# Kernel tuning notes

Measured on AMD Instinct MI355X. Metric: run time of the kernel, lower is better.

## Reference

```python
import jax, jax.numpy as jnp
import numpy as np

B, S, D, E, H, TOPK = 4, 1024, 512, 8, 1536, 2
NORM_EPS = 1e-5

def _ln(x, w, b, eps=1e-5):
    m = jnp.mean(x, -1, keepdims=True)
    v = jnp.var(x, -1, keepdims=True)  # biased var, as torch LayerNorm
    return (x - m) * jax.lax.rsqrt(v + eps) * w + b

def _modulate(x, shift, scale):
    return x * (1 + scale[:, None, :]) + shift[:, None, :]

def setup_inputs() -> dict:
    key = jax.random.key(0)
    ks = jax.random.split(key, 14)
    s = 0.02
    return dict(
        x=jax.random.normal(ks[0], (B, S, D), jnp.float32),
        c=jax.random.normal(ks[1], (B, D), jnp.float32),
        W_ada=jax.random.normal(ks[2], (D, 6 * D), jnp.float32) * s,
        b_ada=jax.random.normal(ks[3], (6 * D,), jnp.float32) * 0.1,
        Wq=jax.random.normal(ks[4], (D, D), jnp.float32) * s,
        Wk=jax.random.normal(ks[5], (D, D), jnp.float32) * s,
        Wv=jax.random.normal(ks[6], (D, D), jnp.float32) * s,
        Wo=jax.random.normal(ks[7], (D, D), jnp.float32) * s,
        qn_w=jnp.ones((D,), jnp.float32), qn_b=jnp.zeros((D,), jnp.float32),
        kn_w=jnp.ones((D,), jnp.float32), kn_b=jnp.zeros((D,), jnp.float32),
        an_w=jnp.ones((D,), jnp.float32), an_b=jnp.zeros((D,), jnp.float32),
        fn_w=jnp.ones((D,), jnp.float32), fn_b=jnp.zeros((D,), jnp.float32),
        Wr=jax.random.normal(ks[8], (D, E), jnp.float32) * s,
        br=jnp.zeros((E,), jnp.float32),
        W1=jax.random.normal(ks[9], (E, D, H), jnp.float32) * s,
        W2=jax.random.normal(ks[10], (E, H, D), jnp.float32) * s,
        W3=jax.random.normal(ks[11], (E, D, H), jnp.float32) * s,
    )

def reference(x, c, W_ada, b_ada, Wq, Wk, Wv, Wo, qn_w, qn_b, kn_w, kn_b,
              an_w, an_b, fn_w, fn_b, Wr, br, W1, W2, W3):
    # adaLN conditioning: SiLU -> Linear -> 6 chunks
    mods = jax.nn.silu(c) @ W_ada + b_ada          # (B, 6D)
    sh_msa, sc_msa, g_msa, sh_mlp, sc_mlp, g_mlp = jnp.split(mods, 6, axis=1)

    # Attention (source attends over the FEATURE dim: scores are (B, D, D))
    h = _modulate(_ln(x, an_w, an_b, NORM_EPS), sh_msa, sc_msa)
    q = _ln(h @ Wq, qn_w, qn_b)
    k = _ln(h @ Wk, kn_w, kn_b)
    v = h @ Wv
    scores = jnp.einsum('bsd,bse->bde', q, k)      # (B, D, D), no 1/sqrt scale (as source)
    A = jax.nn.softmax(scores, axis=-1)
    attn = jnp.einsum('bde,bse->bsd', A, v) @ Wo   # (B, S, D)
    x = x + g_msa[:, None, :] * attn

    # MoE feed-forward (top-2 routing; output REPLACES x, no residual/gate per source)
    xm = _modulate(_ln(x, fn_w, fn_b, NORM_EPS), sh_mlp, sc_mlp)
    logits = xm @ Wr + br                          # (B, S, E)
    # F.normalize default dim=1 -> L2 normalize over the SEQUENCE axis (faithful)
    nrm = jnp.sqrt(jnp.sum(logits * logits, axis=1, keepdims=True))
    logits = logits / jnp.maximum(nrm, 1e-12)
    probs = jax.nn.softmax(logits, axis=-1)        # (B, S, E)
    vals, idx = jax.lax.top_k(probs, TOPK)

    T = B * S
    xf = xm.reshape(T, D)
    # dense combine weights: zero for unselected experts (same math as gather/scatter-add)
    wden = jnp.zeros((T, E), xf.dtype).at[jnp.arange(T)[:, None], idx.reshape(T, TOPK)].set(vals.reshape(T, TOPK))
    h1 = jnp.einsum('td,edh->teh', xf, W1)
    h3 = jnp.einsum('td,edh->teh', xf, W3)
    y = jnp.einsum('teh,ehd->ted', jnp.sin(h1) * h3, W2)  # sin-gated FFN per expert
    moe = jnp.einsum('ted,te->td', y, wden).reshape(B, S, D)

    avg = probs.mean(axis=0)                       # mean over batch dim only (faithful): (S, E)
    aux = jnp.sum((1.0 / E - avg) ** 2)
    return moe, aux
```

## Files before the change

kernel.cpp:

```cpp
#include <hip/hip_runtime.h>
#include <math.h>

#define NB 4
#define NS 1024
#define ND 512
#define NE 8
#define NH 1536
#define NT 4096
#define D6 3072

typedef _Float16 half_t;
typedef _Float16 f16x8 __attribute__((ext_vector_type(8)));
typedef _Float16 f16x4 __attribute__((ext_vector_type(4)));
typedef float    f32x4 __attribute__((ext_vector_type(4)));

#define LDC 136
#define TM_MAX 71

__device__ __forceinline__ void gld16(const void* g, void* l) {
  __builtin_amdgcn_global_load_lds((const __attribute__((address_space(1))) char*)g,
                                   (__attribute__((address_space(3))) char*)l, 16, 0, 0);
}

__device__ __forceinline__ int xcd_chunk(int bid, int nwg) {
  int xcd = bid & 7, ixc = bid >> 3;
  int q = nwg >> 3, r = nwg & 7;
  return (xcd < r ? xcd * (q + 1) : r * (q + 1) + (xcd - r) * q) + ixc;
}

__device__ __forceinline__ int resolve_tile(const int* __restrict__ offs, int t,
                                            int& e_out, int& m0_out) {
  int acc = 0, found = 0, ee = 0, mm = 0;
  #pragma unroll
  for (int q = 0; q < NE; ++q) {
    int ne_q = offs[q + 1] - offs[q];
    int te = (ne_q + 127) >> 7;
    if (!found && t < acc + te) { ee = q; mm = (t - acc) << 7; found = 1; }
    acc += te;
  }
  e_out = ee; m0_out = mm;
  return found;
}

__global__ __launch_bounds__(256) void k_ada(const float* __restrict__ c,
    const float* __restrict__ Wada, const float* __restrict__ bada,
    float* __restrict__ mods)
{
  __shared__ float sc[ND];
  __shared__ float part[256];
  int tid = threadIdx.x;
  int blk = blockIdx.x;
  int o0 = blk * 32;
  int b = o0 / D6;
  int j0 = o0 - b * D6;
  for (int d = tid; d < ND; d += 256) {
    float v = c[b * ND + d];
    sc[d] = v / (1.f + expf(-v));
  }
  __syncthreads();
  int j = j0 + (tid & 31);
  int kc = tid >> 5;
  float acc = 0.f;
  #pragma unroll 8
  for (int d = kc * 64; d < kc * 64 + 64; ++d)
    acc += sc[d] * Wada[(size_t)d * D6 + j];
  part[tid] = acc;
  __syncthreads();
  if (tid < 32) {
    float r = bada[j0 + tid];
    #pragma unroll
    for (int k = 0; k < 8; ++k) r += part[tid + 32 * k];
    mods[b * D6 + j0 + tid] = r;
  }
}

__global__ __launch_bounds__(256) void k_lnmod(const float* X, int xstride,
    float* Yf, half_t* Yh, half_t* Yl, int ystride,
    const float* __restrict__ w, const float* __restrict__ b,
    const float* __restrict__ mods, int sh_off, int sc_off,
    const float* __restrict__ Wr, const float* __restrict__ br,
    float* __restrict__ logits)
{
  __shared__ float red[16];
  __shared__ float red2[32];
  int tid = threadIdx.x;
  int row = blockIdx.x;
  int batch = row >> 10;
  const float* xr = X + (size_t)row * xstride;
  float x0 = xr[tid], x1 = xr[tid + 256];
  float s = x0 + x1, q = x0 * x0 + x1 * x1;
  #pragma unroll
  for (int off = 32; off > 0; off >>= 1) { s += __shfl_down(s, off, 64); q += __shfl_down(q, off, 64); }
  if ((tid & 63) == 0) { red[tid >> 6] = s; red[8 + (tid >> 6)] = q; }
  __syncthreads();
  if (tid == 0) {
    float S = red[0] + red[1] + red[2] + red[3];
    float Q = red[8] + red[9] + red[10] + red[11];
    float mean = S * (1.f / (float)ND);
    float var = Q * (1.f / (float)ND) - mean * mean;
    red[0] = mean; red[1] = rsqrtf(var + 1e-5f);
  }
  __syncthreads();
  float mean = red[0], rstd = red[1];
  int d0 = tid, d1 = tid + 256;
  float y0 = (x0 - mean) * rstd * w[d0] + b[d0];
  float y1 = (x1 - mean) * rstd * w[d1] + b[d1];
  if (mods) {
    const float* mb = mods + batch * D6;
    y0 = y0 * (1.f + mb[sc_off + d0]) + mb[sh_off + d0];
    y1 = y1 * (1.f + mb[sc_off + d1]) + mb[sh_off + d1];
  }
  size_t o0 = (size_t)row * ystride + d0, o1 = (size_t)row * ystride + d1;
  if (Yf) { Yf[o0] = y0; Yf[o1] = y1; }
  if (Yh) {
    half_t h0 = (half_t)y0, h1 = (half_t)y1;
    Yh[o0] = h0; Yh[o1] = h1;
    if (Yl) { Yl[o0] = (half_t)(y0 - (float)h0); Yl[o1] = (half_t)(y1 - (float)h1); }
  }
  if (Wr) {
    float p[8];
    float4 wa = *(const float4*)(Wr + d0 * 8);
    float4 wb = *(const float4*)(Wr + d0 * 8 + 4);
    float4 wc = *(const float4*)(Wr + d1 * 8);
    float4 wd = *(const float4*)(Wr + d1 * 8 + 4);
    p[0] = y0 * wa.x + y1 * wc.x; p[1] = y0 * wa.y + y1 * wc.y;
    p[2] = y0 * wa.z + y1 * wc.z; p[3] = y0 * wa.w + y1 * wc.w;
    p[4] = y0 * wb.x + y1 * wd.x; p[5] = y0 * wb.y + y1 * wd.y;
    p[6] = y0 * wb.z + y1 * wd.z; p[7] = y0 * wb.w + y1 * wd.w;
    #pragma unroll
    for (int off = 32; off > 0; off >>= 1)
      #pragma unroll
      for (int e = 0; e < 8; ++e) p[e] += __shfl_down(p[e], off, 64);
    if ((tid & 63) == 0) {
      #pragma unroll
      for (int e = 0; e < 8; ++e) red2[(tid >> 6) * 8 + e] = p[e];
    }
    __syncthreads();
    if (tid < 8)
      logits[(size_t)row * 8 + tid] = red2[tid] + red2[8 + tid] + red2[16 + tid]
                                    + red2[24 + tid] + br[tid];
  }
}

__global__ __launch_bounds__(256) void k_lnt(const float* __restrict__ QKV,
    const float* __restrict__ qw, const float* __restrict__ qb,
    const float* __restrict__ kw, const float* __restrict__ kb,
    half_t* __restrict__ H0, half_t* __restrict__ L0)
{
  __shared__ float stats[32][2];
  __shared__ float tile[32][33];
  int h = blockIdx.y;
  int s0 = blockIdx.x * 32;
  const float* w = h ? kw : qw;
  const float* b = h ? kb : qb;
  half_t* outH = H0 + (size_t)h * 4194304;
  half_t* outL = L0 + (size_t)h * 4194304;
  int col0 = h * 512;
  int tid = threadIdx.x;
  {
    int r = tid >> 3, c8 = tid & 7;
    const float* xr = QKV + (size_t)(s0 + r) * 1536 + col0 + c8 * 64;
    float s = 0.f, q = 0.f;
    #pragma unroll
    for (int i = 0; i < 16; ++i) {
      float4 v = *(const float4*)(xr + i * 4);
      s += v.x + v.y + v.z + v.w;
      q += v.x * v.x + v.y * v.y + v.z * v.z + v.w * v.w;
    }
    #pragma unroll
    for (int off = 4; off > 0; off >>= 1) {
      s += __shfl_down(s, off, 8);
      q += __shfl_down(q, off, 8);
    }
    if (c8 == 0) {
      float mean = s * (1.f / 512.f);
      float var = q * (1.f / 512.f) - mean * mean;
      stats[r][0] = mean;
      stats[r][1] = rsqrtf(var + 1e-5f);
    }
  }
  __syncthreads();
  int r = tid >> 5, c = tid & 31;
  #pragma unroll 1
  for (int ct = 0; ct < 16; ++ct) {
    int cb = ct * 32;
    #pragma unroll
    for (int p = 0; p < 4; ++p) {
      int rr = r + p * 8;
      float v = QKV[(size_t)(s0 + rr) * 1536 + col0 + cb + c];
      tile[rr][c] = (v - stats[rr][0]) * stats[rr][1] * w[cb + c] + b[cb + c];
    }
    __syncthreads();
    #pragma unroll
    for (int p = 0; p < 4; ++p) {
      int rr = r + p * 8;
      float v = tile[c][rr];
      half_t hh = (half_t)v;
      size_t o = (size_t)(cb + rr) * NT + s0 + c;
      outH[o] = hh;
      outL[o] = (half_t)(v - (float)hh);
    }
    __syncthreads();
  }
}

__global__ __launch_bounds__(256) void k_wsplit4(const float* __restrict__ Wq,
    const float* __restrict__ Wk, const float* __restrict__ Wv,
    const float* __restrict__ Wo, half_t* __restrict__ outH, half_t* __restrict__ outL)
{
  __shared__ float tile[32][33];
  int z = blockIdx.z;
  const float* W = (z == 0) ? Wq : (z == 1) ? Wk : (z == 2) ? Wv : Wo;
  int rowoff = z * 512;
  int k0 = blockIdx.x * 32, n0 = blockIdx.y * 32;
  int tid = threadIdx.x;
  int r = tid >> 5, c = tid & 31;
  #pragma unroll
  for (int p = 0; p < 4; ++p)
    tile[r + p * 8][c] = W[(size_t)(k0 + r + p * 8) * ND + n0 + c];
  __syncthreads();
  #pragma unroll
  for (int p = 0; p < 4; ++p) {
    float v = tile[c][r + p * 8];
    half_t h = (half_t)v;
    size_t o = (size_t)(rowoff + n0 + r + p * 8) * ND + k0 + c;
    outH[o] = h; outL[o] = (half_t)(v - (float)h);
  }
}

template<int MODE>
__global__ __launch_bounds__(256, 2) void k_gemm_hl(
    const half_t* __restrict__ Ah, const half_t* __restrict__ Al, long long sAz,
    const half_t* __restrict__ Bh, const half_t* __restrict__ Bl, long long sBz,
    int lda, int ldb, int K,
    float* __restrict__ Cf, half_t* __restrict__ Ch, half_t* __restrict__ Cl,
    long long sCz, int ldc,
    const float* __restrict__ xres, const float* __restrict__ mods,
    half_t* __restrict__ vh, half_t* __restrict__ vl)
{
  int z = blockIdx.z;
  int m0 = blockIdx.x * 128, n0 = blockIdx.y * 128;
  __shared__ __align__(16) char smem[65536];
  half_t* Sh = (half_t*)smem;
  int tid = threadIdx.x;
  int lane = tid & 63, w = tid >> 6;
  int wm = (w >> 1) * 64, wn = (w & 1) * 64;
  int qd = lane >> 4, md = lane & 15;
  int rA0 = tid >> 2;
  int sw = (((tid & 3) ^ ((tid >> 3) & 3)) << 3);

  const half_t* pAh0 = Ah + z * sAz + (size_t)(m0 + rA0) * lda + sw;
  const half_t* pAh1 = pAh0 + (size_t)64 * lda;
  const half_t* pAl0 = Al + z * sAz + (size_t)(m0 + rA0) * lda + sw;
  const half_t* pAl1 = pAl0 + (size_t)64 * lda;
  const half_t* pBh0 = Bh + z * sBz + (size_t)(n0 + rA0) * ldb + sw;
  const half_t* pBh1 = pBh0 + (size_t)64 * ldb;
  const half_t* pBl0 = Bl + z * sBz + (size_t)(n0 + rA0) * ldb + sw;
  const half_t* pBl1 = pBl0 + (size_t)64 * ldb;

  char* dAh = smem + w * 1024;
  char* dAl = smem + 16384 + w * 1024;
  char* dBh = smem + 32768 + w * 1024;
  char* dBl = smem + 49152 + w * 1024;

  f32x4 acc[4][4];
  #pragma unroll
  for (int i = 0; i < 4; ++i)
    #pragma unroll
    for (int j = 0; j < 4; ++j)
      #pragma unroll
      for (int p = 0; p < 4; ++p) acc[i][j][p] = 0.f;

  int swq  = ((qd ^ ((md >> 1) & 3)) << 3);
  int aoff = (wm + md) * 32 + swq;
  int boff = (wn + md) * 32 + swq;

#define GEMM_STAGE(p, kk) do { int kb_ = (kk); int pb_ = (p) * 8192;         \
    gld16(pAh0 + kb_, dAh + pb_); gld16(pAh1 + kb_, dAh + pb_ + 4096);       \
    gld16(pAl0 + kb_, dAl + pb_); gld16(pAl1 + kb_, dAl + pb_ + 4096);       \
    gld16(pBh0 + kb_, dBh + pb_); gld16(pBh1 + kb_, dBh + pb_ + 4096);       \
    gld16(pBl0 + kb_, dBl + pb_); gld16(pBl1 + kb_, dBl + pb_ + 4096); } while (0)

  int iters = K >> 5;
  GEMM_STAGE(0, 0);
  int cur = 0;
  #pragma unroll 1
  for (int it = 0; it < iters; ++it) {
    if (it + 1 < iters) {
      GEMM_STAGE(cur ^ 1, (it + 1) * 32);
      asm volatile("s_waitcnt vmcnt(8)\ns_barrier" ::: "memory");
    } else {
      asm volatile("s_waitcnt vmcnt(0)\ns_barrier" ::: "memory");
    }
    const half_t* Ash = Sh + cur * 4096;
    const half_t* Asl = Sh + 8192  + cur * 4096;
    const half_t* Bsh = Sh + 16384 + cur * 4096;
    const half_t* Bsl = Sh + 24576 + cur * 4096;
    f16x8 ah[4], al[4], bh[4], bl[4];
    #pragma unroll
    for (int i = 0; i < 4; ++i) {
      ah[i] = *(const f16x8*)(Ash + aoff + i * 512);
      al[i] = *(const f16x8*)(Asl + aoff + i * 512);
    }
    #pragma unroll
    for (int j = 0; j < 4; ++j) {
      bh[j] = *(const f16x8*)(Bsh + boff + j * 512);
      bl[j] = *(const f16x8*)(Bsl + boff + j * 512);
    }
    __builtin_amdgcn_s_setprio(1);
    #pragma unroll
    for (int i = 0; i < 4; ++i)
      #pragma unroll
      for (int j = 0; j < 4; ++j) {
        acc[i][j] = __builtin_amdgcn_mfma_f32_16x16x32_f16(ah[i], bh[j], acc[i][j], 0, 0, 0);
        acc[i][j] = __builtin_amdgcn_mfma_f32_16x16x32_f16(ah[i], bl[j], acc[i][j], 0, 0, 0);
        acc[i][j] = __builtin_amdgcn_mfma_f32_16x16x32_f16(al[i], bh[j], acc[i][j], 0, 0, 0);
      }
    __builtin_amdgcn_s_setprio(0);
    asm volatile("s_barrier" ::: "memory");
    cur ^= 1;
  }
#undef GEMM_STAGE

  if (MODE == 1) {
    half_t* Cs = (half_t*)smem;
    __syncthreads();
    #pragma unroll
    for (int i = 0; i < 4; ++i)
      #pragma unroll
      for (int j = 0; j < 4; ++j)
        #pragma unroll
        for (int p = 0; p < 4; ++p)
          Cs[(wm + 16 * i + qd * 4 + p) * LDC + wn + 16 * j + md] = (half_t)acc[i][j][p];
    __syncthreads();
    #pragma unroll
    for (int it2 = 0; it2 < 8; ++it2) {
      int chunk = it2 * 256 + tid;
      int r = chunk >> 4, c8 = (chunk & 15) * 8;
      *(f16x8*)(Ch + z * sCz + (size_t)(m0 + r) * ldc + n0 + c8) = *(const f16x8*)(Cs + r * LDC + c8);
    }
    __syncthreads();
    #pragma unroll
    for (int i = 0; i < 4; ++i)
      #pragma unroll
      for (int j = 0; j < 4; ++j)
        #pragma unroll
        for (int p = 0; p < 4; ++p) {
          float v = acc[i][j][p];
          half_t h = (half_t)v;
          Cs[(wm + 16 * i + qd * 4 + p) * LDC + wn + 16 * j + md] = (half_t)(v - (float)h);
        }
    __syncthreads();
    #pragma unroll
    for (int it2 = 0; it2 < 8; ++it2) {
      int chunk = it2 * 256 + tid;
      int r = chunk >> 4, c8 = (chunk & 15) * 8;
      *(f16x8*)(Cl + z * sCz + (size_t)(m0 + r) * ldc + n0 + c8) = *(const f16x8*)(Cs + r * LDC + c8);
    }
  } else if (MODE == 3 && n0 >= 1024) {
    #pragma unroll
    for (int i = 0; i < 4; ++i)
      #pragma unroll
      for (int p = 0; p < 4; ++p) {
        int r = m0 + wm + 16 * i + qd * 4 + p;
        int vc = n0 - 1024 + wn + md;
        half_t* hp = vh + (size_t)r * ND + vc;
        half_t* lp = vl + (size_t)r * ND + vc;
        #pragma unroll
        for (int j = 0; j < 4; ++j) {
          float v = acc[i][j][p];
          half_t h = (half_t)v;
          hp[16 * j] = h;
          lp[16 * j] = (half_t)(v - (float)h);
        }
      }
  } else {
    #pragma unroll
    for (int i = 0; i < 4; ++i)
      #pragma unroll
      for (int p = 0; p < 4; ++p) {
        int r = m0 + wm + 16 * i + qd * 4 + p;
        float* cp = Cf + z * sCz + (size_t)r * ldc + n0 + wn + md;
        if (MODE == 2) {
          int batch = r >> 10;
          const float* mb = mods + batch * D6 + 2 * ND;
          const float* xp = xres + (size_t)r * ldc + n0 + wn + md;
          #pragma unroll
          for (int j = 0; j < 4; ++j) {
            int col = wn + md + 16 * j;
            cp[16 * j] = xp[16 * j] + mb[n0 + col] * acc[i][j][p];
          }
        } else {
          #pragma unroll
          for (int j = 0; j < 4; ++j) cp[16 * j] = acc[i][j][p];
        }
      }
  }
}

__global__ __launch_bounds__(256) void k_softmax512_sum4(const float* __restrict__ SC4,
    half_t* __restrict__ Ph, half_t* __restrict__ Pl)
{
  __shared__ float red[16];
  int tid = threadIdx.x;
  int row = blockIdx.x;
  int b = row >> 9, d = row & 511;
  const float* r0 = SC4 + ((size_t)(b * 4 + 0) << 18) + (size_t)d * ND;
  const float* r1 = SC4 + ((size_t)(b * 4 + 1) << 18) + (size_t)d * ND;
  const float* r2 = SC4 + ((size_t)(b * 4 + 2) << 18) + (size_t)d * ND;
  const float* r3 = SC4 + ((size_t)(b * 4 + 3) << 18) + (size_t)d * ND;
  float x0 = r0[tid] + r1[tid] + r2[tid] + r3[tid];
  float x1 = r0[tid + 256] + r1[tid + 256] + r2[tid + 256] + r3[tid + 256];
  float m = fmaxf(x0, x1);
  #pragma unroll
  for (int off = 32; off > 0; off >>= 1) m = fmaxf(m, __shfl_down(m, off, 64));
  if ((tid & 63) == 0) red[tid >> 6] = m;
  __syncthreads();
  if (tid == 0) red[0] = fmaxf(fmaxf(red[0], red[1]), fmaxf(red[2], red[3]));
  __syncthreads();
  m = red[0];
  float e0 = expf(x0 - m), e1 = expf(x1 - m);
  float s = e0 + e1;
  #pragma unroll
  for (int off = 32; off > 0; off >>= 1) s += __shfl_down(s, off, 64);
  if ((tid & 63) == 0) red[8 + (tid >> 6)] = s;
  __syncthreads();
  if (tid == 0) red[8] = red[8] + red[9] + red[10] + red[11];
  __syncthreads();
  float inv = 1.f / red[8];
  float p0 = e0 * inv, p1 = e1 * inv;
  size_t base = (size_t)row * ND;
  half_t h0 = (half_t)p0, h1 = (half_t)p1;
  Ph[base + tid] = h0;       Pl[base + tid] = (half_t)(p0 - (float)h0);
  Ph[base + tid + 256] = h1; Pl[base + tid + 256] = (half_t)(p1 - (float)h1);
}

__global__ __launch_bounds__(256) void k_colnorm(const float* __restrict__ logits,
    float* __restrict__ nrm)
{
  __shared__ float red[8];
  int tid = threadIdx.x;
  int b = blockIdx.x >> 3, e = blockIdx.x & 7;
  float acc = 0.f;
  for (int s = tid; s < NS; s += 256) {
    float l = logits[((size_t)(b << 10) + s) * NE + e];
    acc += l * l;
  }
  #pragma unroll
  for (int off = 32; off > 0; off >>= 1) acc += __shfl_down(acc, off, 64);
  if ((tid & 63) == 0) red[tid >> 6] = acc;
  __syncthreads();
  if (tid == 0) nrm[b * NE + e] = sqrtf(red[0] + red[1] + red[2] + red[3]);
}

__global__ __launch_bounds__(1024) void k_route(const float* __restrict__ logits,
    const float* __restrict__ nrm,
    float* __restrict__ wsel, int* __restrict__ offs_g,
    int* __restrict__ list, int* __restrict__ inv,
    float* __restrict__ outAux)
{
  __shared__ unsigned char sisel[8192];
  __shared__ int cw[8][16][8];
  __shared__ int soffs[9];
  __shared__ float snrm[32];
  __shared__ float auxred[16];
  int tid = threadIdx.x;
  int lane = tid & 63, wv = tid >> 6;
  if (tid < 32) snrm[tid] = fmaxf(nrm[tid], 1e-12f);
  __syncthreads();
  float asum[8];
  #pragma unroll
  for (int e = 0; e < 8; ++e) asum[e] = 0.f;
  #pragma unroll 1
  for (int c = 0; c < 4; ++c) {
    int t = c * 1024 + tid;
    int b = t >> 10;
    float p[8];
    float4 l0 = *(const float4*)(logits + (size_t)t * 8);
    float4 l1 = *(const float4*)(logits + (size_t)t * 8 + 4);
    p[0] = l0.x / snrm[b * 8 + 0]; p[1] = l0.y / snrm[b * 8 + 1];
    p[2] = l0.z / snrm[b * 8 + 2]; p[3] = l0.w / snrm[b * 8 + 3];
    p[4] = l1.x / snrm[b * 8 + 4]; p[5] = l1.y / snrm[b * 8 + 5];
    p[6] = l1.z / snrm[b * 8 + 6]; p[7] = l1.w / snrm[b * 8 + 7];
    float mx = p[0];
    #pragma unroll
    for (int e = 1; e < 8; ++e) mx = fmaxf(mx, p[e]);
    float s = 0.f;
    #pragma unroll
    for (int e = 0; e < 8; ++e) { p[e] = expf(p[e] - mx); s += p[e]; }
    float invs = 1.f / s;
    #pragma unroll
    for (int e = 0; e < 8; ++e) { p[e] *= invs; asum[e] += p[e]; }
    int i1 = 0;
    #pragma unroll
    for (int e = 1; e < 8; ++e) if (p[e] > p[i1]) i1 = e;
    int i2 = (i1 == 0) ? 1 : 0;
    #pragma unroll
    for (int e = 0; e < 8; ++e) if (e != i1 && p[e] > p[i2]) i2 = e;
    wsel[t * 2] = p[i1]; wsel[t * 2 + 1] = p[i2];
    sisel[t * 2] = (unsigned char)i1; sisel[t * 2 + 1] = (unsigned char)i2;
  }
  float aloc = 0.f;
  #pragma unroll
  for (int e = 0; e < 8; ++e) {
    float d = 0.125f - asum[e] * 0.25f;
    aloc += d * d;
  }
  #pragma unroll
  for (int off = 32; off > 0; off >>= 1) aloc += __shfl_down(aloc, off, 64);
  if (lane == 0) auxred[wv] = aloc;
  __syncthreads();
  if (tid == 0) {
    float a = 0.f;
    #pragma unroll
    for (int k = 0; k < 16; ++k) a += auxred[k];
    *outAux = a;
  }
  #pragma unroll 1
  for (int c = 0; c < 8; ++c) {
    int em = sisel[c * 1024 + tid];
    #pragma unroll
    for (int e = 0; e < 8; ++e) {
      unsigned long long mask = __ballot(em == e);
      if (lane == 0) cw[c][wv][e] = (int)__popcll(mask);
    }
  }
  __syncthreads();
  if (tid < 8) {
    int e = tid, run = 0;
    for (int c = 0; c < 8; ++c)
      for (int w2 = 0; w2 < 16; ++w2) { int v = cw[c][w2][e]; cw[c][w2][e] = run; run += v; }
    soffs[e] = run;
  }
  __syncthreads();
  if (tid == 0) {
    int a = 0;
    #pragma unroll
    for (int e = 0; e < 8; ++e) { int v = soffs[e]; soffs[e] = a; a += v; }
    soffs[8] = a;
  }
  __syncthreads();
  if (tid < 9) offs_g[tid] = soffs[tid];
  #pragma unroll 1
  for (int c = 0; c < 8; ++c) {
    int idx = c * 1024 + tid;
    int em = sisel[idx];
    int rk = 0;
    #pragma unroll
    for (int e = 0; e < 8; ++e) {
      unsigned long long mask = __ballot(em == e);
      if (em == e) rk = (int)__popcll(mask & ((1ull << lane) - 1ull));
    }
    int slot = soffs[em] + cw[c][wv][em] + rk;
    list[slot] = idx >> 1;
    inv[idx] = slot;
  }
}

__global__ __launch_bounds__(256) void k_tcast13(const float* __restrict__ W1,
    const float* __restrict__ W3, half_t* __restrict__ W1t, half_t* __restrict__ W3t)
{
  __shared__ float tile[64][68];
  int z = blockIdx.z;
  int sel = z >> 3, e = z & 7;
  const float* We = (sel ? W3 : W1) + (size_t)e * ND * NH;
  half_t* Wte = (sel ? W3t : W1t) + (size_t)e * ND * NH;
  int k0 = blockIdx.x * 64, n0 = blockIdx.y * 64;
  int tid = threadIdx.x;
  int r = tid >> 4, c4 = tid & 15;
  #pragma unroll
  for (int p = 0; p < 4; ++p) {
    int row = r + p * 16;
    float4 v = *(const float4*)(We + (size_t)(k0 + row) * NH + n0 + c4 * 4);
    tile[row][c4 * 4 + 0] = v.x; tile[row][c4 * 4 + 1] = v.y;
    tile[row][c4 * 4 + 2] = v.z; tile[row][c4 * 4 + 3] = v.w;
  }
  __syncthreads();
  #pragma unroll
  for (int p = 0; p < 4; ++p) {
    int orow = r + p * 16;
    f16x4 h;
    #pragma unroll
    for (int i = 0; i < 4; ++i) h[i] = (half_t)tile[c4 * 4 + i][orow];
    *(f16x4*)(Wte + (size_t)(n0 + orow) * ND + k0 + c4 * 4) = h;
  }
}

__global__ __launch_bounds__(256) void k_tcastW2(const float* __restrict__ W,
    half_t* __restrict__ Wt)
{
  __shared__ float tile[64][68];
  const float* We = W + (size_t)blockIdx.z * NH * ND;
  half_t* Wte = Wt + (size_t)blockIdx.z * NH * ND;
  int k0 = blockIdx.x * 64, n0 = blockIdx.y * 64;
  int tid = threadIdx.x;
  int r = tid >> 4, c4 = tid & 15;
  #pragma unroll
  for (int p = 0; p < 4; ++p) {
    int row = r + p * 16;
    float4 v = *(const float4*)(We + (size_t)(k0 + row) * ND + n0 + c4 * 4);
    tile[row][c4 * 4 + 0] = v.x; tile[row][c4 * 4 + 1] = v.y;
    tile[row][c4 * 4 + 2] = v.z; tile[row][c4 * 4 + 3] = v.w;
  }
  __syncthreads();
  #pragma unroll
  for (int p = 0; p < 4; ++p) {
    int orow = r + p * 16;
    f16x4 h;
    #pragma unroll
    for (int i = 0; i < 4; ++i) h[i] = (half_t)tile[c4 * 4 + i][orow];
    *(f16x4*)(Wte + (size_t)(n0 + orow) * NH + k0 + c4 * 4) = h;
  }
}

__global__ __launch_bounds__(256, 3) void k_ffn_fused(const half_t* __restrict__ xmh,
    const half_t* __restrict__ W1t, const half_t* __restrict__ W3t,
    const int* __restrict__ list, const int* __restrict__ offs,
    half_t* __restrict__ gate)
{
  int bx = xcd_chunk(blockIdx.x, TM_MAX * 12);
  int n0 = (bx % 12) * 128;
  int t  = bx / 12;
  int e, m0;
  if (!resolve_tile(offs, t, e, m0)) return;
  int base = offs[e], ne = offs[e + 1] - base;

  __shared__ __align__(16) char smem[49664];
  half_t* Sh = (half_t*)smem;
  int* rowt = (int*)(smem + 49152);
  int tid = threadIdx.x;
  if (tid < 128) {
    int rr = m0 + tid;
    rowt[tid] = (rr < ne) ? list[base + rr] : 0;
  }
  __syncthreads();

  int lane = tid & 63, w = tid >> 6;
  int wm = (w >> 1) * 64, wn = (w & 1) * 64;
  int qd = lane >> 4, md = lane & 15;
  int rA0 = tid >> 2;
  int sw = (((tid & 3) ^ ((tid >> 3) & 3)) << 3);
  int tok0 = rowt[rA0], tok1 = rowt[rA0 + 64];

  const half_t* gA0  = xmh + (size_t)tok0 * ND + sw;
  const half_t* gA1  = xmh + (size_t)tok1 * ND + sw;
  const half_t* gB10 = W1t + ((size_t)e * NH + n0 + rA0) * ND + sw;
  const half_t* gB11 = gB10 + (size_t)64 * ND;
  const half_t* gB30 = W3t + ((size_t)e * NH + n0 + rA0) * ND + sw;
  const half_t* gB31 = gB30 + (size_t)64 * ND;

  char* dA  = smem + w * 1024;
  char* dB1 = smem + 16384 + w * 1024;
  char* dB3 = smem + 32768 + w * 1024;

  f32x4 acc1[4][4], acc3[4][4];
  #pragma unroll
  for (int i = 0; i < 4; ++i)
    #pragma unroll
    for (int j = 0; j < 4; ++j)
      #pragma unroll
      for (int p = 0; p < 4; ++p) { acc1[i][j][p] = 0.f; acc3[i][j][p] = 0.f; }

  int swq  = ((qd ^ ((md >> 1) & 3)) << 3);
  int aoff = (wm + md) * 32 + swq;
  int boff = (wn + md) * 32 + swq;

#define FFN_STAGE(p, kk) do { int kb_ = (kk); int pb_ = (p) * 8192;          \
    gld16(gA0  + kb_, dA  + pb_); gld16(gA1  + kb_, dA  + pb_ + 4096);       \
    gld16(gB10 + kb_, dB1 + pb_); gld16(gB11 + kb_, dB1 + pb_ + 4096);       \
    gld16(gB30 + kb_, dB3 + pb_); gld16(gB31 + kb_, dB3 + pb_ + 4096); } while (0)

  FFN_STAGE(0, 0);
  int cur = 0;
  #pragma unroll 1
  for (int it = 0; it < 16; ++it) {
    if (it + 1 < 16) {
      FFN_STAGE(cur ^ 1, (it + 1) * 32);
      asm volatile("s_waitcnt vmcnt(6)\ns_barrier" ::: "memory");
    } else {
      asm volatile("s_waitcnt vmcnt(0)\ns_barrier" ::: "memory");
    }
    const half_t* As  = Sh + cur * 4096;
    const half_t* B1s = Sh + 8192  + cur * 4096;
    const half_t* B3s = Sh + 16384 + cur * 4096;
    f16x8 a[4];
    #pragma unroll
    for (int i = 0; i < 4; ++i) a[i] = *(const f16x8*)(As + aoff + i * 512);
    __builtin_amdgcn_s_setprio(1);
    #pragma unroll
    for (int j = 0; j < 4; ++j) {
      f16x8 b1 = *(const f16x8*)(B1s + boff + j * 512);
      f16x8 b3 = *(const f16x8*)(B3s + boff + j * 512);
      #pragma unroll
      for (int i = 0; i < 4; ++i) {
        acc1[i][j] = __builtin_amdgcn_mfma_f32_16x16x32_f16(a[i], b1, acc1[i][j], 0, 0, 0);
        acc3[i][j] = __builtin_amdgcn_mfma_f32_16x16x32_f16(a[i], b3, acc3[i][j], 0, 0, 0);
      }
    }
    __builtin_amdgcn_s_setprio(0);
    asm volatile("s_barrier" ::: "memory");
    cur ^= 1;
  }
#undef FFN_STAGE

  half_t* Cs = (half_t*)smem;
  #pragma unroll
  for (int i = 0; i < 4; ++i)
    #pragma unroll
    for (int j = 0; j < 4; ++j)
      #pragma unroll
      for (int p = 0; p < 4; ++p) {
        int rr = wm + 16 * i + qd * 4 + p;
        int cc = wn + 16 * j + md;
        Cs[rr * LDC + cc] = (half_t)(__sinf(acc1[i][j][p]) * acc3[i][j][p]);
      }
  __syncthreads();
  #pragma unroll
  for (int it = 0; it < 8; ++it) {
    int chunk = it * 256 + tid;
    int rr = chunk >> 4, c8 = (chunk & 15) * 8;
    if (m0 + rr < ne) {
      *(f16x8*)(gate + (size_t)(base + m0 + rr) * NH + n0 + c8) = *(const f16x8*)(Cs + rr * LDC + c8);
    }
  }
}

__global__ __launch_bounds__(256, 4) void k_moe2_mfma(const half_t* __restrict__ gate,
    const half_t* __restrict__ W2t, const int* __restrict__ offs,
    float* __restrict__ P)
{
  int bx = xcd_chunk(blockIdx.x, TM_MAX * 4);
  int n0 = (bx & 3) * 128;
  int t = bx >> 2;
  int e, m0;
  if (!resolve_tile(offs, t, e, m0)) return;
  int base = offs[e], ne = offs[e + 1] - base;

  __shared__ __align__(16) char smem[32768];
  half_t* Sh = (half_t*)smem;
  int tid = threadIdx.x;
  int lane = tid & 63, w = tid >> 6;
  int wm = (w >> 1) * 64, wn = (w & 1) * 64;
  int qd = lane >> 4, md = lane & 15;
  int rA0 = tid >> 2;
  int sw = (((tid & 3) ^ ((tid >> 3) & 3)) << 3);

  int ar0 = m0 + rA0;      if (ar0 >= ne) ar0 = ne - 1;
  int ar1 = m0 + rA0 + 64; if (ar1 >= ne) ar1 = ne - 1;
  const half_t* gA0 = gate + (size_t)(base + ar0) * NH + sw;
  const half_t* gA1 = gate + (size_t)(base + ar1) * NH + sw;
  const half_t* gB0 = W2t + ((size_t)e * ND + n0 + rA0) * NH + sw;
  const half_t* gB1 = gB0 + (size_t)64 * NH;

  char* dA = smem + w * 1024;
  char* dB = smem + 16384 + w * 1024;

  f32x4 acc[4][4];
  #pragma unroll
  for (int i = 0; i < 4; ++i)
    #pragma unroll
    for (int j = 0; j < 4; ++j)
      #pragma unroll
      for (int p = 0; p < 4; ++p) acc[i][j][p] = 0.f;

  int swq  = ((qd ^ ((md >> 1) & 3)) << 3);
  int aoff = (wm + md) * 32 + swq;
  int boff = (wn + md) * 32 + swq;

#define MOE2_STAGE(p, kk) do { int kb_ = (kk); int pb_ = (p) * 8192;         \
    gld16(gA0 + kb_, dA + pb_); gld16(gA1 + kb_, dA + pb_ + 4096);           \
    gld16(gB0 + kb_, dB + pb_); gld16(gB1 + kb_, dB + pb_ + 4096); } while (0)

  MOE2_STAGE(0, 0);
  int cur = 0;
  #pragma unroll 1
  for (int it = 0; it < 48; ++it) {
    if (it + 1 < 48) {
      MOE2_STAGE(cur ^ 1, (it + 1) * 32);
      asm volatile("s_waitcnt vmcnt(4)\ns_barrier" ::: "memory");
    } else {
      asm volatile("s_waitcnt vmcnt(0)\ns_barrier" ::: "memory");
    }
    const half_t* As = Sh + cur * 4096;
    const half_t* Bs = Sh + 8192 + cur * 4096;
    f16x8 a[4], b[4];
    #pragma unroll
    for (int i = 0; i < 4; ++i) a[i] = *(const f16x8*)(As + aoff + i * 512);
    #pragma unroll
    for (int j = 0; j < 4; ++j) b[j] = *(const f16x8*)(Bs + boff + j * 512);
    __builtin_amdgcn_s_setprio(1);
    #pragma unroll
    for (int j = 0; j < 4; ++j)
      #pragma unroll
      for (int i = 0; i < 4; ++i)
        acc[i][j] = __builtin_amdgcn_mfma_f32_16x16x32_f16(a[i], b[j], acc[i][j], 0, 0, 0);
    __builtin_amdgcn_s_setprio(0);
    asm volatile("s_barrier" ::: "memory");
    cur ^= 1;
  }
#undef MOE2_STAGE

  #pragma unroll
  for (int i = 0; i < 4; ++i)
    #pragma unroll
    for (int p = 0; p < 4; ++p) {
      int gr = m0 + wm + 16 * i + qd * 4 + p;
      if (gr < ne) {
        float* pp = P + (size_t)(base + gr) * ND + n0 + wn + md;
        #pragma unroll
        for (int j = 0; j < 4; ++j)
          pp[16 * j] = acc[i][j][p];
      }
    }
}

__global__ __launch_bounds__(256) void k_moe_reduce(const float* __restrict__ P,
    const int* __restrict__ inv, const float* __restrict__ wsel,
    float* __restrict__ out)
{
  int i = blockIdx.x * 256 + threadIdx.x;
  int t = i >> 7, d4 = i & 127;
  int s1 = inv[t * 2], s2 = inv[t * 2 + 1];
  float w1 = wsel[t * 2], w2 = wsel[t * 2 + 1];
  const float4* P4 = (const float4*)P;
  float4 a = P4[(size_t)s1 * 128 + d4];
  float4 b = P4[(size_t)s2 * 128 + d4];
  float4 o;
  o.x = w1 * a.x + w2 * b.x;
  o.y = w1 * a.y + w2 * b.y;
  o.z = w1 * a.z + w2 * b.z;
  o.w = w1 * a.w + w2 * b.w;
  ((float4*)out)[i] = o;
}

static const size_t BO_MODS  = 0;
static const size_t BO_HH    = 65536;
static const size_t BO_HL2   = 4259840;
static const size_t BO_PH    = 4259840;
static const size_t BO_PL    = 6357056;
static const size_t BO_WALLH = 8454144;
static const size_t BO_WALLL = 10551296;
static const size_t BO_QKV   = 12648448;
static const size_t BO_A0H   = 12648448;
static const size_t BO_A0L   = 16842752;
static const size_t BO_SC4   = 21037056;
static const size_t BO_X2    = 21037056;
static const size_t BO_XM    = 29425664;
static const size_t BO_QTH   = 37814272;
static const size_t BO_QTL   = 42008576;
static const size_t BO_KTH   = 46202880;
static const size_t BO_KTL   = 50397184;
static const size_t BO_VH    = 54591488;
static const size_t BO_VL    = 58785792;
static const size_t BO_W1T   = 37814272;
static const size_t BO_XMH   = 50397184;
static const size_t BO_W3T   = 65536;
static const size_t BO_GATE  = 12648448;
static const size_t BO_W2T   = 65536;
static const size_t BO_P     = 37814272;
static const size_t BO_LOGI  = 62980096;
static const size_t BO_NRM   = 63111168;
static const size_t BO_WSEL  = 63242368;
static const size_t BO_INTS  = 63307904;

extern "C" void kernel_launch(void* const* d_in, const int* in_sizes, int n_in,
                              void* d_out, int out_size, void* d_ws, size_t ws_size,
                              hipStream_t stream)
{
  const float* x    = (const float*)d_in[0];
  const float* c    = (const float*)d_in[1];
  const float* Wada = (const float*)d_in[2];
  const float* bada = (const float*)d_in[3];
  const float* Wq   = (const float*)d_in[4];
  const float* Wk   = (const float*)d_in[5];
  const float* Wv   = (const float*)d_in[6];
  const float* Wo   = (const float*)d_in[7];
  const float* qn_w = (const float*)d_in[8];
  const float* qn_b = (const float*)d_in[9];
  const float* kn_w = (const float*)d_in[10];
  const float* kn_b = (const float*)d_in[11];
  const float* an_w = (const float*)d_in[12];
  const float* an_b = (const float*)d_in[13];
  const float* fn_w = (const float*)d_in[14];
  const float* fn_b = (const float*)d_in[15];
  const float* Wr   = (const float*)d_in[16];
  const float* br   = (const float*)d_in[17];
  const float* W1   = (const float*)d_in[18];
  const float* W2   = (const float*)d_in[19];
  const float* W3   = (const float*)d_in[20];
  float* out = (float*)d_out;
  char*  ws8 = (char*)d_ws;
  float* MODS = (float*)(ws8 + BO_MODS);
  half_t* Hh = (half_t*)(ws8 + BO_HH),   *Hl = (half_t*)(ws8 + BO_HL2);
  half_t* Ph = (half_t*)(ws8 + BO_PH),   *Pl = (half_t*)(ws8 + BO_PL);
  half_t* WALLH = (half_t*)(ws8 + BO_WALLH), *WALLL = (half_t*)(ws8 + BO_WALLL);
  half_t* WoTh = WALLH + (size_t)1536 * ND,  *WoTl = WALLL + (size_t)1536 * ND;
  float* QKV = (float*)(ws8 + BO_QKV);
  half_t* A0h = (half_t*)(ws8 + BO_A0H), *A0l = (half_t*)(ws8 + BO_A0L);
  float* SC4 = (float*)(ws8 + BO_SC4);
  float* X2  = (float*)(ws8 + BO_X2);
  half_t* qTh = (half_t*)(ws8 + BO_QTH), *qTl = (half_t*)(ws8 + BO_QTL);
  half_t* kTh = (half_t*)(ws8 + BO_KTH), *kTl = (half_t*)(ws8 + BO_KTL);
  half_t* Vh  = (half_t*)(ws8 + BO_VH),  *Vl  = (half_t*)(ws8 + BO_VL);
  half_t* W1T = (half_t*)(ws8 + BO_W1T);
  half_t* W3T = (half_t*)(ws8 + BO_W3T);
  half_t* W2T = (half_t*)(ws8 + BO_W2T);
  half_t* XMH = (half_t*)(ws8 + BO_XMH);
  half_t* GATEH = (half_t*)(ws8 + BO_GATE);
  float* PBUF = (float*)(ws8 + BO_P);
  float* LOGI = (float*)(ws8 + BO_LOGI);
  float* NRM  = (float*)(ws8 + BO_NRM);
  float* WSEL = (float*)(ws8 + BO_WSEL);
  int* ib   = (int*)(ws8 + BO_INTS);
  int* offs = ib + 8208;
  int* list = ib + 8224;
  int* inv  = ib + 16416;

  k_ada<<<384, 256, 0, stream>>>(c, Wada, bada, MODS);
  k_wsplit4<<<dim3(16, 16, 4), 256, 0, stream>>>(Wq, Wk, Wv, Wo, WALLH, WALLL);
  k_lnmod<<<NT, 256, 0, stream>>>(x, ND, nullptr, Hh, Hl, ND, an_w, an_b, MODS, 0, 512,
                                  nullptr, nullptr, nullptr);
  k_gemm_hl<3><<<dim3(32, 12, 1), 256, 0, stream>>>(Hh, Hl, 0, WALLH, WALLL, 0,
      ND, ND, ND, QKV, nullptr, nullptr, 0, 1536, nullptr, nullptr, Vh, Vl);
  k_lnt<<<dim3(128, 2), 256, 0, stream>>>(QKV, qn_w, qn_b, kn_w, kn_b, qTh, qTl);
  k_gemm_hl<0><<<dim3(4, 4, 16), 256, 0, stream>>>(qTh, qTl, 256, kTh, kTl, 256,
      NT, NT, 256, SC4, nullptr, nullptr, 262144, ND, nullptr, nullptr, nullptr, nullptr);
  k_softmax512_sum4<<<2048, 256, 0, stream>>>(SC4, Ph, Pl);
  k_gemm_hl<1><<<dim3(8, 4, 4), 256, 0, stream>>>(Vh, Vl, 524288, Ph, Pl, 262144,
      ND, ND, ND, nullptr, A0h, A0l, 524288, ND, nullptr, nullptr, nullptr, nullptr);
  k_gemm_hl<2><<<dim3(32, 4, 1), 256, 0, stream>>>(A0h, A0l, 0, WoTh, WoTl, 0,
      ND, ND, ND, X2, nullptr, nullptr, 0, ND, x, MODS, nullptr, nullptr);
  k_lnmod<<<NT, 256, 0, stream>>>(X2, ND, nullptr, XMH, nullptr, ND, fn_w, fn_b, MODS, 1536, 2048,
                                  Wr, br, LOGI);
  k_colnorm<<<32, 256, 0, stream>>>(LOGI, NRM);
  k_route<<<1, 1024, 0, stream>>>(LOGI, NRM, WSEL, offs, list, inv,
                                  out + (size_t)NT * ND);
  k_tcast13<<<dim3(8, 24, 16), 256, 0, stream>>>(W1, W3, W1T, W3T);
  k_ffn_fused<<<TM_MAX * 12, 256, 0, stream>>>(XMH, W1T, W3T, list, offs, GATEH);
  k_tcastW2<<<dim3(24, 8, 8), 256, 0, stream>>>(W2, W2T);
  k_moe2_mfma<<<TM_MAX * 4, 256, 0, stream>>>(GATEH, W2T, offs, PBUF);
  k_moe_reduce<<<2048, 256, 0, stream>>>(PBUF, inv, WSEL, out);
}
```

Baseline: 378.9 us.

## Split scores GEMM into 8 K-slices and fold column norm into router

The split-K factor of the q^T k scores GEMM goes from 4 to 8 (K chunk 128, grid z 32), so more workgroups run in parallel. The softmax kernel now sums 8 partial slabs. The separate column-norm kernel is removed and its sum of squares is computed inside the single-block router using wave shuffles and shared memory, which saves one launch. In exchange the partial-score buffer and the softmax read traffic double, and the router's single block does extra reduction work.

```diff
diff --git a/kernel.cpp b/kernel.cpp
--- a/kernel.cpp
+++ b/kernel.cpp
@@ -398,19 +398,20 @@
   }
 }
 
-__global__ __launch_bounds__(256) void k_softmax512_sum4(const float* __restrict__ SC4,
+__global__ __launch_bounds__(256) void k_softmax512_sum8(const float* __restrict__ SC8,
     half_t* __restrict__ Ph, half_t* __restrict__ Pl)
 {
   __shared__ float red[16];
   int tid = threadIdx.x;
   int row = blockIdx.x;
   int b = row >> 9, d = row & 511;
-  const float* r0 = SC4 + ((size_t)(b * 4 + 0) << 18) + (size_t)d * ND;
-  const float* r1 = SC4 + ((size_t)(b * 4 + 1) << 18) + (size_t)d * ND;
-  const float* r2 = SC4 + ((size_t)(b * 4 + 2) << 18) + (size_t)d * ND;
-  const float* r3 = SC4 + ((size_t)(b * 4 + 3) << 18) + (size_t)d * ND;
-  float x0 = r0[tid] + r1[tid] + r2[tid] + r3[tid];
-  float x1 = r0[tid + 256] + r1[tid + 256] + r2[tid + 256] + r3[tid + 256];
+  float x0 = 0.f, x1 = 0.f;
+  #pragma unroll
+  for (int j = 0; j < 8; ++j) {
+    const float* rj = SC8 + ((size_t)(b * 8 + j) << 18) + (size_t)d * ND;
+    x0 += rj[tid];
+    x1 += rj[tid + 256];
+  }
   float m = fmaxf(x0, x1);
   #pragma unroll
   for (int off = 32; off > 0; off >>= 1) m = fmaxf(m, __shfl_down(m, off, 64));
@@ -435,26 +436,7 @@
   Ph[base + tid + 256] = h1; Pl[base + tid + 256] = (half_t)(p1 - (float)h1);
 }
 
-__global__ __launch_bounds__(256) void k_colnorm(const float* __restrict__ logits,
-    float* __restrict__ nrm)
-{
-  __shared__ float red[8];
-  int tid = threadIdx.x;
-  int b = blockIdx.x >> 3, e = blockIdx.x & 7;
-  float acc = 0.f;
-  for (int s = tid; s < NS; s += 256) {
-    float l = logits[((size_t)(b << 10) + s) * NE + e];
-    acc += l * l;
-  }
-  #pragma unroll
-  for (int off = 32; off > 0; off >>= 1) acc += __shfl_down(acc, off, 64);
-  if ((tid & 63) == 0) red[tid >> 6] = acc;
-  __syncthreads();
-  if (tid == 0) nrm[b * NE + e] = sqrtf(red[0] + red[1] + red[2] + red[3]);
-}
-
 __global__ __launch_bounds__(1024) void k_route(const float* __restrict__ logits,
-    const float* __restrict__ nrm,
     float* __restrict__ wsel, int* __restrict__ offs_g,
     int* __restrict__ list, int* __restrict__ inv,
     float* __restrict__ outAux)
@@ -464,10 +446,44 @@
   __shared__ int soffs[9];
   __shared__ float snrm[32];
   __shared__ float auxred[16];
+  __shared__ float red3[16][32];
   int tid = threadIdx.x;
   int lane = tid & 63, wv = tid >> 6;
-  if (tid < 32) snrm[tid] = fmaxf(nrm[tid], 1e-12f);
-  __syncthreads();
+  {
+    float sq[4][8];
+    #pragma unroll
+    for (int c = 0; c < 4; ++c) {
+      int t = c * 1024 + tid;
+      float4 l0 = *(const float4*)(logits + (size_t)t * 8);
+      float4 l1 = *(const float4*)(logits + (size_t)t * 8 + 4);
+      sq[c][0] = l0.x * l0.x; sq[c][1] = l0.y * l0.y;
+      sq[c][2] = l0.z * l0.z; sq[c][3] = l0.w * l0.w;
+      sq[c][4] = l1.x * l1.x; sq[c][5] = l1.y * l1.y;
+      sq[c][6] = l1.z * l1.z; sq[c][7] = l1.w * l1.w;
+    }
+    #pragma unroll
+    for (int off = 32; off > 0; off >>= 1)
+      #pragma unroll
+      for (int c = 0; c < 4; ++c)
+        #pragma unroll
+        for (int e = 0; e < 8; ++e)
+          sq[c][e] += __shfl_down(sq[c][e], off, 64);
+    if (lane == 0) {
+      #pragma unroll
+      for (int c = 0; c < 4; ++c)
+        #pragma unroll
+        for (int e = 0; e < 8; ++e)
+          red3[wv][c * 8 + e] = sq[c][e];
+    }
+    __syncthreads();
+    if (tid < 32) {
+      float a = 0.f;
+      #pragma unroll
+      for (int k2 = 0; k2 < 16; ++k2) a += red3[k2][tid];
+      snrm[tid] = fmaxf(sqrtf(a), 1e-12f);
+    }
+    __syncthreads();
+  }
   float asum[8];
   #pragma unroll
   for (int e = 0; e < 8; ++e) asum[e] = 0.f;
@@ -843,9 +859,7 @@
 static const size_t BO_QKV   = 12648448;
 static const size_t BO_A0H   = 12648448;
 static const size_t BO_A0L   = 16842752;
-static const size_t BO_SC4   = 21037056;
 static const size_t BO_X2    = 21037056;
-static const size_t BO_XM    = 29425664;
 static const size_t BO_QTH   = 37814272;
 static const size_t BO_QTL   = 42008576;
 static const size_t BO_KTH   = 46202880;
@@ -859,9 +873,9 @@
 static const size_t BO_W2T   = 65536;
 static const size_t BO_P     = 37814272;
 static const size_t BO_LOGI  = 62980096;
-static const size_t BO_NRM   = 63111168;
 static const size_t BO_WSEL  = 63242368;
 static const size_t BO_INTS  = 63307904;
+static const size_t BO_SC8   = 67108864;
 
 extern "C" void kernel_launch(void* const* d_in, const int* in_sizes, int n_in,
                               void* d_out, int out_size, void* d_ws, size_t ws_size,
@@ -897,7 +911,7 @@
   half_t* WoTh = WALLH + (size_t)1536 * ND,  *WoTl = WALLL + (size_t)1536 * ND;
   float* QKV = (float*)(ws8 + BO_QKV);
   half_t* A0h = (half_t*)(ws8 + BO_A0H), *A0l = (half_t*)(ws8 + BO_A0L);
-  float* SC4 = (float*)(ws8 + BO_SC4);
+  float* SC8 = (float*)(ws8 + BO_SC8);
   float* X2  = (float*)(ws8 + BO_X2);
   half_t* qTh = (half_t*)(ws8 + BO_QTH), *qTl = (half_t*)(ws8 + BO_QTL);
   half_t* kTh = (half_t*)(ws8 + BO_KTH), *kTl = (half_t*)(ws8 + BO_KTL);
@@ -909,12 +923,11 @@
   half_t* GATEH = (half_t*)(ws8 + BO_GATE);
   float* PBUF = (float*)(ws8 + BO_P);
   float* LOGI = (float*)(ws8 + BO_LOGI);
-  float* NRM  = (float*)(ws8 + BO_NRM);
   float* WSEL = (float*)(ws8 + BO_WSEL);
   int* ib   = (int*)(ws8 + BO_INTS);
-  int* offs = ib + 8208;
-  int* list = ib + 8224;
-  int* inv  = ib + 16416;
+  int* offs = ib;
+  int* list = ib + 16;
+  int* inv  = ib + 16 + 8192;
 
   k_ada<<<384, 256, 0, stream>>>(c, Wada, bada, MODS);
   k_wsplit4<<<dim3(16, 16, 4), 256, 0, stream>>>(Wq, Wk, Wv, Wo, WALLH, WALLL);
@@ -923,17 +936,16 @@
   k_gemm_hl<3><<<dim3(32, 12, 1), 256, 0, stream>>>(Hh, Hl, 0, WALLH, WALLL, 0,
       ND, ND, ND, QKV, nullptr, nullptr, 0, 1536, nullptr, nullptr, Vh, Vl);
   k_lnt<<<dim3(128, 2), 256, 0, stream>>>(QKV, qn_w, qn_b, kn_w, kn_b, qTh, qTl);
-  k_gemm_hl<0><<<dim3(4, 4, 16), 256, 0, stream>>>(qTh, qTl, 256, kTh, kTl, 256,
-      NT, NT, 256, SC4, nullptr, nullptr, 262144, ND, nullptr, nullptr, nullptr, nullptr);
-  k_softmax512_sum4<<<2048, 256, 0, stream>>>(SC4, Ph, Pl);
+  k_gemm_hl<0><<<dim3(4, 4, 32), 256, 0, stream>>>(qTh, qTl, 128, kTh, kTl, 128,
+      NT, NT, 128, SC8, nullptr, nullptr, 262144, ND, nullptr, nullptr, nullptr, nullptr);
+  k_softmax512_sum8<<<2048, 256, 0, stream>>>(SC8, Ph, Pl);
   k_gemm_hl<1><<<dim3(8, 4, 4), 256, 0, stream>>>(Vh, Vl, 524288, Ph, Pl, 262144,
       ND, ND, ND, nullptr, A0h, A0l, 524288, ND, nullptr, nullptr, nullptr, nullptr);
   k_gemm_hl<2><<<dim3(32, 4, 1), 256, 0, stream>>>(A0h, A0l, 0, WoTh, WoTl, 0,
       ND, ND, ND, X2, nullptr, nullptr, 0, ND, x, MODS, nullptr, nullptr);
   k_lnmod<<<NT, 256, 0, stream>>>(X2, ND, nullptr, XMH, nullptr, ND, fn_w, fn_b, MODS, 1536, 2048,
                                   Wr, br, LOGI);
-  k_colnorm<<<32, 256, 0, stream>>>(LOGI, NRM);
-  k_route<<<1, 1024, 0, stream>>>(LOGI, NRM, WSEL, offs, list, inv,
+  k_route<<<1, 1024, 0, stream>>>(LOGI, WSEL, offs, list, inv,
                                   out + (size_t)NT * ND);
   k_tcast13<<<dim3(8, 24, 16), 256, 0, stream>>>(W1, W3, W1T, W3T);
   k_ffn_fused<<<TM_MAX * 12, 256, 0, stream>>>(XMH, W1T, W3T, list, offs, GATEH);
```

After: 395.5 us. +4.4%, slower.
